# Kernel optimization log

Measured on AMD Instinct MI355X. Metric: run time of the kernel, lower is better.

Reference implementation:

```python
import jax, jax.numpy as jnp
import numpy as np


def _scan_dir(x, Wih, Whh, b, reverse):
    # x: (B,T,D); Wih: (4H,D); Whh: (4H,H); b: (4H,)  (= b_ih+b_hh)
    B = x.shape[0]
    H = Whh.shape[1]
    xg = jnp.einsum('btd,gd->btg', x, Wih) + b          # (B,T,4H) precomputed input projections
    xg = jnp.swapaxes(xg, 0, 1)                          # (T,B,4H)

    def step(carry, g_t):
        h, c = carry
        g = g_t + h @ Whh.T
        i, f, gg, o = jnp.split(g, 4, axis=-1)           # PyTorch gate order: i,f,g,o
        c = jax.nn.sigmoid(f) * c + jax.nn.sigmoid(i) * jnp.tanh(gg)
        h = jax.nn.sigmoid(o) * jnp.tanh(c)
        return (h, c), h

    h0 = jnp.zeros((B, H), x.dtype)
    _, hs = jax.lax.scan(step, (h0, h0), xg, reverse=reverse)
    return jnp.swapaxes(hs, 0, 1)                        # (B,T,H), time order preserved


def _bilstm(x, Wih_f, Whh_f, b_f, Wih_b, Whh_b, b_b):
    out_f = _scan_dir(x, Wih_f, Whh_f, b_f, reverse=False)
    out_b = _scan_dir(x, Wih_b, Whh_b, b_b, reverse=True)
    return jnp.concatenate([out_f, out_b], axis=-1)      # (B,T,2H)


def setup_inputs() -> dict:
    key = jax.random.key(0)
    ks = iter(jax.random.split(key, 32))
    B, T = 1024, 128
    H1, H2 = 50, 150

    def p(shape, scale):
        return (jax.random.normal(next(ks), shape, dtype=jnp.float32) * scale)

    s1 = 1.0 / np.sqrt(H1)
    s2 = 1.0 / np.sqrt(H2)
    inp = {
        'x': jax.random.normal(next(ks), (B, 1, T), dtype=jnp.float32),
        'rrs': jax.random.normal(next(ks), (B, 4), dtype=jnp.float32),
        # layer 1: in_dim=1, H=50, bidirectional
        'l1_Wih_f': p((4 * H1, 1), s1), 'l1_Whh_f': p((4 * H1, H1), s1), 'l1_b_f': p((4 * H1,), s1),
        'l1_Wih_b': p((4 * H1, 1), s1), 'l1_Whh_b': p((4 * H1, H1), s1), 'l1_b_b': p((4 * H1,), s1),
        # layer 2: in_dim=100, H=150, bidirectional
        'l2_Wih_f': p((4 * H2, 2 * H1), s2), 'l2_Whh_f': p((4 * H2, H2), s2), 'l2_b_f': p((4 * H2,), s2),
        'l2_Wih_b': p((4 * H2, 2 * H1), s2), 'l2_Whh_b': p((4 * H2, H2), s2), 'l2_b_b': p((4 * H2,), s2),
        # heads
        'head_W': p((20, 2 * H2), 0.05), 'head_b': p((20,), 0.05),
        'pef1_W': p((10, 4), 0.05), 'pef1_b': p((10,), 0.05),
        'pef2_W': p((2, 10), 0.05), 'pef2_b': p((2,), 0.05),
        'fc_W': p((4, 30), 0.05), 'fc_b': p((4,), 0.05),
    }
    return inp


def reference(x, rrs,
              l1_Wih_f, l1_Whh_f, l1_b_f, l1_Wih_b, l1_Whh_b, l1_b_b,
              l2_Wih_f, l2_Whh_f, l2_b_f, l2_Wih_b, l2_Whh_b, l2_b_b,
              head_W, head_b, pef1_W, pef1_b, pef2_W, pef2_b, fc_W, fc_b):
    xt = jnp.transpose(x, (0, 2, 1))                     # (B,T,1)
    out1 = _bilstm(xt, l1_Wih_f, l1_Whh_f, l1_b_f, l1_Wih_b, l1_Whh_b, l1_b_b)   # (B,T,100)
    out2 = _bilstm(out1, l2_Wih_f, l2_Whh_f, l2_b_f, l2_Wih_b, l2_Whh_b, l2_b_b) # (B,T,300)
    net = out2[:, -1]                                    # (B,300)
    waveform_feat = jax.nn.leaky_relu(net @ head_W.T + head_b, 0.3)              # (B,20)
    pef = jax.nn.leaky_relu(rrs @ pef1_W.T + pef1_b, 0.3)                        # (B,10)
    pef_logits = pef @ pef2_W.T + pef2_b                                         # (B,2)
    feat = jnp.concatenate([waveform_feat, pef], axis=1)                         # (B,30)
    logits = feat @ fc_W.T + fc_b                                                # (B,4)
    return (waveform_feat, pef_logits, feat, logits)
```

## Files before the change

### kernel.cpp

```cpp
#include <hip/hip_runtime.h>


typedef unsigned short u16;
typedef unsigned int u32;
typedef float f32x4 __attribute__((ext_vector_type(4)));
typedef _Float16 f16x8 __attribute__((ext_vector_type(8)));
typedef short s16x8 __attribute__((ext_vector_type(8)));

#if __has_builtin(__builtin_amdgcn_mfma_f32_16x16x32_f16)
#define USE_F16 1
#else
#define USE_F16 0
#endif

#define B1 1024
#define TT 128

__device__ __forceinline__ u16 to_h(float x) {
#if USE_F16
    _Float16 h = (_Float16)x;
    return __builtin_bit_cast(u16, h);
#else
    u32 u = __builtin_bit_cast(u32, x);
    u32 r = u + 0x7FFFu + ((u >> 16) & 1u);
    return (u16)(r >> 16);
#endif
}
__device__ __forceinline__ float from_h(u16 s) {
#if USE_F16
    return (float)__builtin_bit_cast(_Float16, s);
#else
    u32 u = ((u32)s) << 16;
    return __builtin_bit_cast(float, u);
#endif
}

__device__ __forceinline__ f32x4 mfma16(uint4 a, uint4 b, f32x4 c) {
#if USE_F16
    return __builtin_amdgcn_mfma_f32_16x16x32_f16(
        __builtin_bit_cast(f16x8, a), __builtin_bit_cast(f16x8, b), c, 0, 0, 0);
#else
    return __builtin_amdgcn_mfma_f32_16x16x32_bf16(
        __builtin_bit_cast(s16x8, a), __builtin_bit_cast(s16x8, b), c, 0, 0, 0);
#endif
}

#define LOG2E 1.4426950408889634f
__device__ __forceinline__ float sigm(float x) {
    return __builtin_amdgcn_rcpf(1.f + __builtin_amdgcn_exp2f(-LOG2E * x));
}
__device__ __forceinline__ float tanh_(float x) {
    return 1.f - 2.f * __builtin_amdgcn_rcpf(1.f + __builtin_amdgcn_exp2f(2.f * LOG2E * x));
}

__global__ void prep_frag(const float* __restrict__ Wih, const float* __restrict__ Whh,
                          const float* __restrict__ bias, uint4* __restrict__ dst,
                          int GR, int NW, int NP, int KT,
                          int x_off, int x_len, int h_off, int h_len, int bias_k)
{
    int bid = blockIdx.x;
    int l = threadIdx.x;
    int tile = bid / KT, kt = bid - tile * KT;
    int ml = l & 15;
    int qq = ml >> 2, tau = ml & 3;
    int w = tile % NW, p = tile / NW;
    int jj = (w * 4 + qq) * NP + p;
    bool valid = jj < GR;
    int row = tau * GR + jj;
    u32 dw[4];
    #pragma unroll
    for (int d = 0; d < 4; ++d) {
        u16 hh[2];
        #pragma unroll
        for (int s = 0; s < 2; ++s) {
            int j = d * 2 + s;
            int k = kt * 32 + (l >> 4) * 8 + j;
            float val = 0.f;
            if (valid) {
                if (k >= x_off && k < x_off + x_len) val = Wih[row * x_len + (k - x_off)];
                else if (k >= h_off && k < h_off + h_len) val = Whh[row * h_len + (k - h_off)];
                else if (k == bias_k) val = bias[row];
            }
            hh[s] = to_h(val);
        }
        dw[d] = (u32)hh[0] | ((u32)hh[1] << 16);
    }
    uint4 o; o.x = dw[0]; o.y = dw[1]; o.z = dw[2]; o.w = dw[3];
    dst[bid * 64 + l] = o;
}

__global__ void prep_transT(const float* __restrict__ W, float* __restrict__ WtT, int K, int G)
{
    int idx = blockIdx.x * 256 + threadIdx.x;
    if (idx < K * G) {
        int k = idx / G, g = idx - k * G;
        WtT[idx] = W[g * K + k];
    }
}

__global__ __launch_bounds__(256, 4) void l1_scan(
    const float* __restrict__ x, const uint4* __restrict__ fragF,
    const uint4* __restrict__ fragB, u16* __restrict__ out1f)
{
    const int tid = threadIdx.x;
    const int lane = tid & 63;
    const int w = tid >> 6;
    const int q = lane >> 4;
    const int b = lane & 15;
    const int blk = blockIdx.x;
    const int dir = blockIdx.y;
    const uint4* frag = dir ? fragB : fragF;

    __shared__ u16 v[2][1024];
    __shared__ float x_s[128][17];

    uint4 af[4][2];
    #pragma unroll
    for (int i = 0; i < 4; ++i)
        #pragma unroll
        for (int kt = 0; kt < 2; ++kt)
            af[i][kt] = frag[((w + 4 * i) * 2 + kt) * 64 + lane];

    const int b0 = blk * 16;
    for (int idx = tid; idx < 1024; idx += 256) ((u32*)v)[idx] = 0u;
    for (int idx = tid; idx < 2048; idx += 256) {
        int bb = idx >> 7, t = idx & 127;
        x_s[t][bb] = x[(size_t)(b0 + bb) * TT + t];
    }
    __syncthreads();
    const u16 oneh = to_h(1.0f);
    if (tid < 16) {
        v[0][(112 + tid) * 8 + 7] = oneh;
        v[1][(112 + tid) * 8 + 7] = oneh;
        v[0][tid * 8] = to_h(x[(size_t)(b0 + tid) * TT + (dir ? TT - 1 : 0)]);
    }
    const int jjb = w * 16 + q * 4;
    int vslot[4]; size_t eb[4];
    #pragma unroll
    for (int p = 0; p < 4; ++p) {
        int jj = jjb + p;
        int k = 1 + jj;
        vslot[p] = ((k >> 5) * 64 + ((k & 31) >> 3) * 16 + b) * 8 + (k & 7);
        int k2 = dir * 50 + jj;
        eb[p] = (((size_t)blk * 4 + (k2 >> 5)) * 64 + ((k2 & 31) >> 3) * 16 + b) * 8 + (k2 & 7);
    }
    float c[4] = {0.f, 0.f, 0.f, 0.f};
    __syncthreads();

#define L1_STEP(T, CUR) { \
    uint4 bf0 = *(const uint4*)&v[CUR][lane * 8]; \
    uint4 bf1 = *(const uint4*)&v[CUR][(64 + lane) * 8]; \
    f32x4 acc[4]; \
    _Pragma("unroll") for (int i = 0; i < 4; ++i) acc[i] = (f32x4){0.f, 0.f, 0.f, 0.f}; \
    _Pragma("unroll") for (int i = 0; i < 4; ++i) acc[i] = mfma16(af[i][0], bf0, acc[i]); \
    _Pragma("unroll") for (int i = 0; i < 4; ++i) acc[i] = mfma16(af[i][1], bf1, acc[i]); \
    const int tt = dir ? 127 - (T) : (T); \
    _Pragma("unroll") for (int p = 0; p < 4; ++p) { \
        if (jjb + p < 50) { \
            float ig = acc[p][0], fg = acc[p][1], gg = acc[p][2], og = acc[p][3]; \
            float cn = sigm(fg) * c[p] + sigm(ig) * tanh_(gg); \
            float hn = sigm(og) * tanh_(cn); \
            c[p] = cn; \
            u16 hb = to_h(hn); \
            out1f[eb[p] + (size_t)tt * 131072] = hb; \
            v[1 - (CUR)][vslot[p]] = hb; \
        } \
    } \
    if (tid < 16 && (T) < 127) \
        v[1 - (CUR)][tid * 8] = to_h(x_s[dir ? 126 - (T) : (T) + 1][tid]); \
    __syncthreads(); }

    for (int t2 = 0; t2 < TT; t2 += 2) {
        L1_STEP(t2, 0)
        L1_STEP(t2 + 1, 1)
    }
#undef L1_STEP
}

__global__ __launch_bounds__(512, 2) void l2f_scan(
    const uint4* __restrict__ frag, const u16* __restrict__ out1f,
    float* __restrict__ net)
{
    const int tid = threadIdx.x;
    const int lane = tid & 63;
    const int w = tid >> 6;
    const int q = lane >> 4;
    const int b = lane & 15;
    const int blk = blockIdx.x;
    const int b0 = blk * 16;
    const uint4* o4 = (const uint4*)out1f;

    __shared__ u16 v[2][4096];

    uint4 af[5][8];
    #pragma unroll
    for (int i = 0; i < 5; ++i)
        #pragma unroll
        for (int kt = 0; kt < 8; ++kt)
            af[i][kt] = frag[((w + 8 * i) * 8 + kt) * 64 + lane];

    for (int idx = tid; idx < 4096; idx += 512) ((u32*)v)[idx] = 0u;

    uint4 pfA[4], pfB[4];
    #pragma unroll
    for (int ktx = 0; ktx < 4; ++ktx)
        pfA[ktx] = o4[((size_t)blk * 4 + ktx) * 64 + lane];

    __syncthreads();
    const u16 oneh = to_h(1.0f);
    if (tid < 16) {
        v[0][(496 + tid) * 8 + 7] = oneh;
        v[1][(496 + tid) * 8 + 7] = oneh;
    }
    if (w == 0 && lane < 16) {
        uint2 xv; xv.x = pfA[3].x; xv.y = pfA[3].y;
        *(uint2*)&v[0][(192 + lane) * 8] = xv;
    }

    const int jjb = w * 20 + q * 5;
    int vslot[5];
    #pragma unroll
    for (int p = 0; p < 5; ++p) {
        int k = 100 + jjb + p;
        vslot[p] = ((k >> 5) * 64 + ((k & 31) >> 3) * 16 + b) * 8 + (k & 7);
    }
    float c[5] = {0.f, 0.f, 0.f, 0.f, 0.f};
    __syncthreads();

#define L2F_STEP(T, CUR, PFC, PFN) { \
    const int tn = ((T) < 127) ? (T) + 1 : 127; \
    _Pragma("unroll") for (int ktx = 0; ktx < 4; ++ktx) \
        PFN[ktx] = o4[(((size_t)tn * 64 + blk) * 4 + ktx) * 64 + lane]; \
    uint4 bfu[5]; \
    _Pragma("unroll") for (int kh = 0; kh < 5; ++kh) \
        bfu[kh] = *(const uint4*)&v[CUR][((kh + 3) * 64 + lane) * 8]; \
    f32x4 acc[5]; \
    _Pragma("unroll") for (int i = 0; i < 5; ++i) acc[i] = (f32x4){0.f, 0.f, 0.f, 0.f}; \
    _Pragma("unroll") for (int kt = 0; kt < 3; ++kt) { \
        _Pragma("unroll") for (int i = 0; i < 5; ++i) \
            acc[i] = mfma16(af[i][kt], PFC[kt], acc[i]); } \
    _Pragma("unroll") for (int kh = 0; kh < 5; ++kh) { \
        _Pragma("unroll") for (int i = 0; i < 5; ++i) \
            acc[i] = mfma16(af[i][kh + 3], bfu[kh], acc[i]); } \
    _Pragma("unroll") for (int p = 0; p < 5; ++p) { \
        float ig = acc[p][0], fg = acc[p][1], gg = acc[p][2], og = acc[p][3]; \
        float cn = sigm(fg) * c[p] + sigm(ig) * tanh_(gg); \
        float hn = sigm(og) * tanh_(cn); \
        c[p] = cn; \
        if (jjb + p < 150) { \
            v[1 - (CUR)][vslot[p]] = to_h(hn); \
            if ((T) == 127) net[(size_t)(b0 + b) * 300 + jjb + p] = hn; \
        } \
    } \
    if (w == 0 && lane < 16) { \
        uint2 xv; xv.x = PFN[3].x; xv.y = PFN[3].y; \
        *(uint2*)&v[1 - (CUR)][(192 + lane) * 8] = xv; \
    } \
    __syncthreads(); }

    for (int t2 = 0; t2 < TT; t2 += 2) {
        L2F_STEP(t2, 0, pfA, pfB)
        L2F_STEP(t2 + 1, 1, pfB, pfA)
    }
#undef L2F_STEP
}

__global__ __launch_bounds__(640, 1) void l2b_step(
    const u16* __restrict__ out1f, const float* __restrict__ WtT,
    const float* __restrict__ bias, float* __restrict__ net)
{
    const int tid = threadIdx.x;
    const int blk = blockIdx.x;
    const int b0 = blk * 16;
    __shared__ alignas(16) float x_s[100][16];
    __shared__ alignas(16) float gbuf[16][644];
    for (int idx = tid; idx < 1600; idx += 640) {
        int k2 = idx >> 4, bb = idx & 15;
        x_s[k2][bb] = from_h(out1f[((((size_t)127 * 64 + blk) * 4 + (k2 >> 5)) * 64
                                    + ((k2 & 31) >> 3) * 16 + bb) * 8 + (k2 & 7)]);
    }
    __syncthreads();
    if (tid < 600) {
        int g = tid;
        float acc[16];
        #pragma unroll
        for (int bb = 0; bb < 16; ++bb) acc[bb] = 0.f;
        for (int k = 0; k < 100; ++k) {
            float wv = WtT[k * 600 + g];
            float4 xa = *(const float4*)&x_s[k][0];
            float4 xb = *(const float4*)&x_s[k][4];
            float4 xc = *(const float4*)&x_s[k][8];
            float4 xd = *(const float4*)&x_s[k][12];
            acc[0] = fmaf(wv, xa.x, acc[0]);  acc[1] = fmaf(wv, xa.y, acc[1]);
            acc[2] = fmaf(wv, xa.z, acc[2]);  acc[3] = fmaf(wv, xa.w, acc[3]);
            acc[4] = fmaf(wv, xb.x, acc[4]);  acc[5] = fmaf(wv, xb.y, acc[5]);
            acc[6] = fmaf(wv, xb.z, acc[6]);  acc[7] = fmaf(wv, xb.w, acc[7]);
            acc[8] = fmaf(wv, xc.x, acc[8]);  acc[9] = fmaf(wv, xc.y, acc[9]);
            acc[10] = fmaf(wv, xc.z, acc[10]); acc[11] = fmaf(wv, xc.w, acc[11]);
            acc[12] = fmaf(wv, xd.x, acc[12]); acc[13] = fmaf(wv, xd.y, acc[13]);
            acc[14] = fmaf(wv, xd.z, acc[14]); acc[15] = fmaf(wv, xd.w, acc[15]);
        }
        #pragma unroll
        for (int bb = 0; bb < 16; ++bb) gbuf[bb][g] = acc[bb];
    }
    __syncthreads();
    for (int idx = tid; idx < 2400; idx += 640) {
        int j = idx >> 4, bb = idx & 15;
        float ig = gbuf[bb][j]       + bias[j];
        float gg = gbuf[bb][j + 300] + bias[j + 300];
        float og = gbuf[bb][j + 450] + bias[j + 450];
        float cn = sigm(ig) * tanh_(gg);
        float hn = sigm(og) * tanh_(cn);
        net[(size_t)(b0 + bb) * 300 + 150 + j] = hn;
    }
}

__global__ void head1(const float* __restrict__ net, const float* __restrict__ rrs,
                      const float* __restrict__ headW, const float* __restrict__ headb,
                      const float* __restrict__ p1W, const float* __restrict__ p1b,
                      const float* __restrict__ p2W, const float* __restrict__ p2b,
                      float* __restrict__ out)
{
    int gid = blockIdx.x * 256 + threadIdx.x;
    int b = gid >> 2, og = gid & 3;
    float acc[5];
    #pragma unroll
    for (int o2 = 0; o2 < 5; ++o2) acc[o2] = headb[og * 5 + o2];
    const float* nb = net + (size_t)b * 300;
    for (int k = 0; k < 300; ++k) {
        float nv = nb[k];
        #pragma unroll
        for (int o2 = 0; o2 < 5; ++o2)
            acc[o2] = fmaf(headW[(og * 5 + o2) * 300 + k], nv, acc[o2]);
    }
    #pragma unroll
    for (int o2 = 0; o2 < 5; ++o2) {
        int o = og * 5 + o2;
        float vv = acc[o2] > 0.f ? acc[o2] : 0.3f * acc[o2];
        out[b * 20 + o] = vv;
        out[22528 + b * 30 + o] = vv;
    }
    if (og == 0) {
        float p[10];
        #pragma unroll
        for (int r = 0; r < 10; ++r) {
            float a = p1b[r];
            #pragma unroll
            for (int qq = 0; qq < 4; ++qq) a = fmaf(p1W[r * 4 + qq], rrs[b * 4 + qq], a);
            p[r] = a > 0.f ? a : 0.3f * a;
            out[22528 + b * 30 + 20 + r] = p[r];
        }
        #pragma unroll
        for (int s = 0; s < 2; ++s) {
            float a = p2b[s];
            #pragma unroll
            for (int r = 0; r < 10; ++r) a = fmaf(p2W[s * 10 + r], p[r], a);
            out[20480 + b * 2 + s] = a;
        }
    }
}

__global__ void head2(const float* __restrict__ fcW, const float* __restrict__ fcb,
                      float* __restrict__ out)
{
    int b = blockIdx.x * 256 + threadIdx.x;
    const float* feat = out + 22528 + b * 30;
    float f[30];
    #pragma unroll
    for (int k = 0; k < 30; ++k) f[k] = feat[k];
    #pragma unroll
    for (int s = 0; s < 4; ++s) {
        float a = fcb[s];
        #pragma unroll
        for (int k = 0; k < 30; ++k) a = fmaf(fcW[s * 30 + k], f[k], a);
        out[53248 + b * 4 + s] = a;
    }
}

extern "C" void kernel_launch(void* const* d_in, const int* in_sizes, int n_in,
                              void* d_out, int out_size, void* d_ws, size_t ws_size,
                              hipStream_t stream)
{
    const float* x     = (const float*)d_in[0];
    const float* rrs   = (const float*)d_in[1];
    const float* W1ihF = (const float*)d_in[2];
    const float* W1hhF = (const float*)d_in[3];
    const float* b1F   = (const float*)d_in[4];
    const float* W1ihB = (const float*)d_in[5];
    const float* W1hhB = (const float*)d_in[6];
    const float* b1B   = (const float*)d_in[7];
    const float* W2ihF = (const float*)d_in[8];
    const float* W2hhF = (const float*)d_in[9];
    const float* b2F   = (const float*)d_in[10];
    const float* W2ihB = (const float*)d_in[11];
    const float* b2B   = (const float*)d_in[13];
    const float* headW = (const float*)d_in[14];
    const float* headb = (const float*)d_in[15];
    const float* p1W   = (const float*)d_in[16];
    const float* p1b   = (const float*)d_in[17];
    const float* p2W   = (const float*)d_in[18];
    const float* p2b   = (const float*)d_in[19];
    const float* fcW   = (const float*)d_in[20];
    const float* fcb   = (const float*)d_in[21];
    float* out = (float*)d_out;

    char* ws = (char*)d_ws;
    uint4* frag1f = (uint4*)(ws + 0);
    uint4* frag1b = (uint4*)(ws + 32768);
    uint4* frag2f = (uint4*)(ws + 65536);
    float* WtT    = (float*)(ws + 393216);
    u16*   out1f  = (u16*)(ws + 655360);
    float* net    = (float*)(ws + 655360 + 33554432);
    (void)ws_size; (void)in_sizes; (void)n_in; (void)out_size;

    prep_frag<<<32, 64, 0, stream>>>(W1ihF, W1hhF, b1F, frag1f, 50, 4, 4, 2, 0, 1, 1, 50, 63);
    prep_frag<<<32, 64, 0, stream>>>(W1ihB, W1hhB, b1B, frag1b, 50, 4, 4, 2, 0, 1, 1, 50, 63);
    prep_frag<<<320, 64, 0, stream>>>(W2ihF, W2hhF, b2F, frag2f, 150, 8, 5, 8, 0, 100, 100, 150, 255);
    prep_transT<<<(60000 + 255) / 256, 256, 0, stream>>>(W2ihB, WtT, 100, 600);
    l1_scan<<<dim3(64, 2), 256, 0, stream>>>(x, frag1f, frag1b, out1f);
    l2f_scan<<<64, 512, 0, stream>>>(frag2f, out1f, net);
    l2b_step<<<64, 640, 0, stream>>>(out1f, WtT, b2B, net);
    head1<<<16, 256, 0, stream>>>(net, rrs, headW, headb, p1W, p1b, p2W, p2b, out);
    head2<<<4, 256, 0, stream>>>(fcW, fcb, out);
}
```

Measured before the change: 322.2 us.

## Merge prep kernels, widen layer-1 scan to 8 waves, lighten per-step barriers

```diff
diff --git a/kernel.cpp b/kernel.cpp
--- a/kernel.cpp
+++ b/kernel.cpp
@@ -53,13 +53,19 @@
     return 1.f - 2.f * __builtin_amdgcn_rcpf(1.f + __builtin_amdgcn_exp2f(2.f * LOG2E * x));
 }
 
-__global__ void prep_frag(const float* __restrict__ Wih, const float* __restrict__ Whh,
-                          const float* __restrict__ bias, uint4* __restrict__ dst,
-                          int GR, int NW, int NP, int KT,
-                          int x_off, int x_len, int h_off, int h_len, int bias_k)
-{
-    int bid = blockIdx.x;
-    int l = threadIdx.x;
+__device__ __forceinline__ void wg_barrier_lds() {
+    __builtin_amdgcn_sched_barrier(0);
+    asm volatile("s_waitcnt lgkmcnt(0)" ::: "memory");
+    __builtin_amdgcn_s_barrier();
+    __builtin_amdgcn_sched_barrier(0);
+}
+
+__device__ __forceinline__ void prep_frag_body(
+    const float* __restrict__ Wih, const float* __restrict__ Whh,
+    const float* __restrict__ bias, uint4* __restrict__ dst,
+    int GR, int NW, int NP, int KT,
+    int x_off, int x_len, int h_off, int h_len, int bias_k, int bid, int l)
+{
     int tile = bid / KT, kt = bid - tile * KT;
     int ml = l & 15;
     int qq = ml >> 2, tau = ml & 3;
@@ -89,16 +95,33 @@
     dst[bid * 64 + l] = o;
 }
 
-__global__ void prep_transT(const float* __restrict__ W, float* __restrict__ WtT, int K, int G)
-{
-    int idx = blockIdx.x * 256 + threadIdx.x;
-    if (idx < K * G) {
-        int k = idx / G, g = idx - k * G;
-        WtT[idx] = W[g * K + k];
-    }
-}
-
-__global__ __launch_bounds__(256, 4) void l1_scan(
+__global__ void prep_all(const float* __restrict__ W1ihF, const float* __restrict__ W1hhF,
+                         const float* __restrict__ b1F,
+                         const float* __restrict__ W1ihB, const float* __restrict__ W1hhB,
+                         const float* __restrict__ b1B,
+                         const float* __restrict__ W2ihF, const float* __restrict__ W2hhF,
+                         const float* __restrict__ b2F, const float* __restrict__ W2ihB,
+                         uint4* __restrict__ frag1f, uint4* __restrict__ frag1b,
+                         uint4* __restrict__ frag2f, float* __restrict__ WtT)
+{
+    int bid = blockIdx.x;
+    int l = threadIdx.x;
+    if (bid < 32)
+        prep_frag_body(W1ihF, W1hhF, b1F, frag1f, 50, 8, 2, 2, 0, 1, 1, 50, 63, bid, l);
+    else if (bid < 64)
+        prep_frag_body(W1ihB, W1hhB, b1B, frag1b, 50, 8, 2, 2, 0, 1, 1, 50, 63, bid - 32, l);
+    else if (bid < 384)
+        prep_frag_body(W2ihF, W2hhF, b2F, frag2f, 150, 8, 5, 8, 0, 100, 100, 150, 255, bid - 64, l);
+    else {
+        int idx = (bid - 384) * 64 + l;
+        if (idx < 60000) {
+            int k = idx / 600, g = idx - k * 600;
+            WtT[idx] = W2ihB[g * 100 + k];
+        }
+    }
+}
+
+__global__ __launch_bounds__(512, 2) void l1_scan(
     const float* __restrict__ x, const uint4* __restrict__ fragF,
     const uint4* __restrict__ fragB, u16* __restrict__ out1f)
 {
@@ -114,16 +137,16 @@
     __shared__ u16 v[2][1024];
     __shared__ float x_s[128][17];
 
-    uint4 af[4][2];
-    #pragma unroll
-    for (int i = 0; i < 4; ++i)
+    uint4 af[2][2];
+    #pragma unroll
+    for (int i = 0; i < 2; ++i)
         #pragma unroll
         for (int kt = 0; kt < 2; ++kt)
-            af[i][kt] = frag[((w + 4 * i) * 2 + kt) * 64 + lane];
+            af[i][kt] = frag[((w + 8 * i) * 2 + kt) * 64 + lane];
 
     const int b0 = blk * 16;
-    for (int idx = tid; idx < 1024; idx += 256) ((u32*)v)[idx] = 0u;
-    for (int idx = tid; idx < 2048; idx += 256) {
+    for (int idx = tid; idx < 1024; idx += 512) ((u32*)v)[idx] = 0u;
+    for (int idx = tid; idx < 2048; idx += 512) {
         int bb = idx >> 7, t = idx & 127;
         x_s[t][bb] = x[(size_t)(b0 + bb) * TT + t];
     }
@@ -134,28 +157,28 @@
         v[1][(112 + tid) * 8 + 7] = oneh;
         v[0][tid * 8] = to_h(x[(size_t)(b0 + tid) * TT + (dir ? TT - 1 : 0)]);
     }
-    const int jjb = w * 16 + q * 4;
-    int vslot[4]; size_t eb[4];
-    #pragma unroll
-    for (int p = 0; p < 4; ++p) {
+    const int jjb = (w * 4 + q) * 2;
+    int vslot[2]; size_t eb[2];
+    #pragma unroll
+    for (int p = 0; p < 2; ++p) {
         int jj = jjb + p;
         int k = 1 + jj;
         vslot[p] = ((k >> 5) * 64 + ((k & 31) >> 3) * 16 + b) * 8 + (k & 7);
         int k2 = dir * 50 + jj;
         eb[p] = (((size_t)blk * 4 + (k2 >> 5)) * 64 + ((k2 & 31) >> 3) * 16 + b) * 8 + (k2 & 7);
     }
-    float c[4] = {0.f, 0.f, 0.f, 0.f};
+    float c[2] = {0.f, 0.f};
     __syncthreads();
 
 #define L1_STEP(T, CUR) { \
     uint4 bf0 = *(const uint4*)&v[CUR][lane * 8]; \
     uint4 bf1 = *(const uint4*)&v[CUR][(64 + lane) * 8]; \
-    f32x4 acc[4]; \
-    _Pragma("unroll") for (int i = 0; i < 4; ++i) acc[i] = (f32x4){0.f, 0.f, 0.f, 0.f}; \
-    _Pragma("unroll") for (int i = 0; i < 4; ++i) acc[i] = mfma16(af[i][0], bf0, acc[i]); \
-    _Pragma("unroll") for (int i = 0; i < 4; ++i) acc[i] = mfma16(af[i][1], bf1, acc[i]); \
+    f32x4 acc[2]; \
+    _Pragma("unroll") for (int i = 0; i < 2; ++i) acc[i] = (f32x4){0.f, 0.f, 0.f, 0.f}; \
+    _Pragma("unroll") for (int i = 0; i < 2; ++i) acc[i] = mfma16(af[i][0], bf0, acc[i]); \
+    _Pragma("unroll") for (int i = 0; i < 2; ++i) acc[i] = mfma16(af[i][1], bf1, acc[i]); \
     const int tt = dir ? 127 - (T) : (T); \
-    _Pragma("unroll") for (int p = 0; p < 4; ++p) { \
+    _Pragma("unroll") for (int p = 0; p < 2; ++p) { \
         if (jjb + p < 50) { \
             float ig = acc[p][0], fg = acc[p][1], gg = acc[p][2], og = acc[p][3]; \
             float cn = sigm(fg) * c[p] + sigm(ig) * tanh_(gg); \
@@ -168,7 +191,7 @@
     } \
     if (tid < 16 && (T) < 127) \
         v[1 - (CUR)][tid * 8] = to_h(x_s[dir ? 126 - (T) : (T) + 1][tid]); \
-    __syncthreads(); }
+    wg_barrier_lds(); }
 
     for (int t2 = 0; t2 < TT; t2 += 2) {
         L1_STEP(t2, 0)
@@ -212,12 +235,9 @@
         v[0][(496 + tid) * 8 + 7] = oneh;
         v[1][(496 + tid) * 8 + 7] = oneh;
     }
-    if (w == 0 && lane < 16) {
-        uint2 xv; xv.x = pfA[3].x; xv.y = pfA[3].y;
-        *(uint2*)&v[0][(192 + lane) * 8] = xv;
-    }
-
-    const int jjb = w * 20 + q * 5;
+
+    const u32 umask = (q == 0) ? 0xFFFFFFFFu : 0u;
+    const int jjb = (w * 4 + q) * 5;
     int vslot[5];
     #pragma unroll
     for (int p = 0; p < 5; ++p) {
@@ -234,6 +254,8 @@
     uint4 bfu[5]; \
     _Pragma("unroll") for (int kh = 0; kh < 5; ++kh) \
         bfu[kh] = *(const uint4*)&v[CUR][((kh + 3) * 64 + lane) * 8]; \
+    bfu[0].x |= PFC[3].x & umask; \
+    bfu[0].y |= PFC[3].y & umask; \
     f32x4 acc[5]; \
     _Pragma("unroll") for (int i = 0; i < 5; ++i) acc[i] = (f32x4){0.f, 0.f, 0.f, 0.f}; \
     _Pragma("unroll") for (int kt = 0; kt < 3; ++kt) { \
@@ -252,11 +274,7 @@
             if ((T) == 127) net[(size_t)(b0 + b) * 300 + jjb + p] = hn; \
         } \
     } \
-    if (w == 0 && lane < 16) { \
-        uint2 xv; xv.x = PFN[3].x; xv.y = PFN[3].y; \
-        *(uint2*)&v[1 - (CUR)][(192 + lane) * 8] = xv; \
-    } \
-    __syncthreads(); }
+    wg_barrier_lds(); }
 
     for (int t2 = 0; t2 < TT; t2 += 2) {
         L2F_STEP(t2, 0, pfA, pfB)
@@ -413,11 +431,10 @@
     float* net    = (float*)(ws + 655360 + 33554432);
     (void)ws_size; (void)in_sizes; (void)n_in; (void)out_size;
 
-    prep_frag<<<32, 64, 0, stream>>>(W1ihF, W1hhF, b1F, frag1f, 50, 4, 4, 2, 0, 1, 1, 50, 63);
-    prep_frag<<<32, 64, 0, stream>>>(W1ihB, W1hhB, b1B, frag1b, 50, 4, 4, 2, 0, 1, 1, 50, 63);
-    prep_frag<<<320, 64, 0, stream>>>(W2ihF, W2hhF, b2F, frag2f, 150, 8, 5, 8, 0, 100, 100, 150, 255);
-    prep_transT<<<(60000 + 255) / 256, 256, 0, stream>>>(W2ihB, WtT, 100, 600);
-    l1_scan<<<dim3(64, 2), 256, 0, stream>>>(x, frag1f, frag1b, out1f);
+    prep_all<<<1322, 64, 0, stream>>>(W1ihF, W1hhF, b1F, W1ihB, W1hhB, b1B,
+                                      W2ihF, W2hhF, b2F, W2ihB,
+                                      frag1f, frag1b, frag2f, WtT);
+    l1_scan<<<dim3(64, 2), 512, 0, stream>>>(x, frag1f, frag1b, out1f);
     l2f_scan<<<64, 512, 0, stream>>>(frag2f, out1f, net);
     l2b_step<<<64, 640, 0, stream>>>(out1f, WtT, b2B, net);
     head1<<<16, 256, 0, stream>>>(net, rrs, headW, headb, p1W, p1b, p2W, p2b, out);
```

Result: faster. 295.4 us (-8.3%).
